# Kernel optimization log

Measured on AMD Instinct MI355X. Metric: run time of the kernel, lower is better.

Reference implementation:

```python
import jax, jax.numpy as jnp
import numpy as np


def setup_inputs() -> dict:
    key = jax.random.key(0)
    ks = jax.random.split(key, 5)
    B, S, D, E, H = 8, 4096, 512, 4, 64
    x = jax.random.normal(ks[0], (B, S, D), dtype=jnp.float32)
    router_w = jax.random.normal(ks[1], (D, E), dtype=jnp.float32) * 0.02
    router_b = jnp.zeros((E,), dtype=jnp.float32)
    w1 = jax.random.normal(ks[2], (E, D, H), dtype=jnp.float32) * 0.02
    b1 = jnp.zeros((E, H), dtype=jnp.float32)
    w2 = jax.random.normal(ks[3], (E, H, D), dtype=jnp.float32) * 0.02
    b2 = jnp.zeros((E, D), dtype=jnp.float32)
    return {"x": x, "router_w": router_w, "router_b": router_b,
            "w1": w1, "b1": b1, "w2": w2, "b2": b2}


def reference(x, router_w, router_b, w1, b1, w2, b2):
    # Router: softmax over experts. weights: [B, S, E]
    weights = jax.nn.softmax(jnp.einsum('bsd,de->bse', x, router_w) + router_b, axis=-1)
    # All experts run densely on every token (batched over the E axis).
    # h: [B, S, E, H]; TF Dense(activation='gelu') uses exact (non-tanh) gelu.
    h = jax.nn.gelu(jnp.einsum('bsd,edh->bseh', x, w1) + b1, approximate=False)
    # expert outputs: [B, S, E, D]; Dropout is identity at inference.
    expert_out = jnp.einsum('bseh,ehd->bsed', h, w2) + b2
    # weighted sum over experts -> [B, S, D]
    return jnp.sum(expert_out * weights[..., None], axis=2)
```

## Files before the change

kernel.cpp:

```cpp
#include <hip/hip_runtime.h>
#include <hip/hip_bf16.h>
#include <math.h>


typedef short v8s  __attribute__((ext_vector_type(8)));
typedef float v16f __attribute__((ext_vector_type(16)));

#define XS 520
#define HS 296

__device__ __forceinline__ unsigned short f2bf(float f) {
    unsigned int u = __builtin_bit_cast(unsigned int, f);
    u += 0x7fffu + ((u >> 16) & 1u);
    return (unsigned short)(u >> 16);
}
__device__ __forceinline__ float gelu_fast(float v) {
    float s  = v * 0.70710678118f;
    float xa = fabsf(s);
    float t  = 1.0f / (1.0f + 0.3275911f * xa);
    float poly = t * (0.254829592f + t * (-0.284496736f + t * (1.421413741f +
                 t * (-1.453152027f + t * 1.061405429f))));
    float er = copysignf(1.0f - poly * __expf(-xa * xa), s);
    return 0.5f * v * (1.0f + er);
}

__global__ void moe_prep(const float* __restrict__ w1,
                         const float* __restrict__ w2,
                         const float* __restrict__ b2,
                         const float* __restrict__ rw,
                         unsigned short* __restrict__ w1p,
                         unsigned short* __restrict__ w2p,
                         unsigned short* __restrict__ rp) {
    int idx = blockIdx.x * 256 + threadIdx.x;
    if (idx < 131072) {
        int block = idx >> 9, within = idx & 511;
        int kstep = block >> 3, cb = block & 7;
        int n = within >> 4, kl = within & 15;
        int k = kstep * 16 + kl;
        int col = cb * 32 + n;
        int e = col >> 6, h = col & 63;
        w1p[idx] = f2bf(w1[(e * 512 + k) * 64 + h]);
    } else if (idx < 131072 + 147456) {
        int op = idx - 131072;
        int block = op >> 9, within = op & 511;
        int kstep = block >> 4, cb = block & 15;
        int n = within >> 4, kl = within & 15;
        int k = kstep * 16 + kl;
        int d = cb * 32 + n;
        float v = 0.f;
        if (k < 256) {
            int e = k >> 6, h = k & 63;
            v = w2[(e * 64 + h) * 512 + d];
        } else if (k < 260) {
            v = b2[(k - 256) * 512 + d];
        }
        w2p[op] = f2bf(v);
    } else if (idx < 131072 + 147456 + 16384) {
        int op = idx - (131072 + 147456);
        int kstep = op >> 9, within = op & 511;
        int n = within >> 4, kl = within & 15;
        int k = kstep * 16 + kl;
        float v = (n < 4) ? rw[k * 4 + n] : 0.f;
        rp[op] = f2bf(v);
    }
}

__global__ __launch_bounds__(256, 2)
void moe_main(const float* __restrict__ x,
              const float* __restrict__ rb,
              const float* __restrict__ b1,
              const unsigned short* __restrict__ w1p,
              const unsigned short* __restrict__ w2p,
              const unsigned short* __restrict__ rp,
              float* __restrict__ out) {
    __shared__ __align__(16) unsigned short lx[64 * XS];
    __shared__ float lw[64 * 4];

    const int tid  = threadIdx.x;
    const int lane = tid & 63, wv = tid >> 6;
    const int ln = lane & 31, hi = lane >> 5;
    const long t0 = (long)blockIdx.x * 64;

    const float4* xt = (const float4*)(x + t0 * 512);
    #pragma unroll
    for (int it = 0; it < 32; ++it) {
        int F = it * 256 + tid;
        int row = F >> 7, c4 = F & 127;
        float4 v = xt[F];
        unsigned int p0 = (unsigned int)f2bf(v.x) | ((unsigned int)f2bf(v.y) << 16);
        unsigned int p1 = (unsigned int)f2bf(v.z) | ((unsigned int)f2bf(v.w) << 16);
        *(uint2*)&lx[row * XS + c4 * 4] = make_uint2(p0, p1);
    }
    __syncthreads();

    v16f acc1[2][2];
    v16f accR;
    #pragma unroll
    for (int j = 0; j < 16; ++j) accR[j] = 0.f;
    #pragma unroll
    for (int mt = 0; mt < 2; ++mt)
        #pragma unroll
        for (int nt = 0; nt < 2; ++nt)
            #pragma unroll
            for (int j = 0; j < 16; ++j) acc1[mt][nt][j] = 0.f;

    const unsigned short* w1b = w1p + (size_t)(wv * 2) * 512 + ln * 16 + hi * 8;
    const unsigned short* rpb = rp + ln * 16 + hi * 8;

    for (int ks = 0; ks < 32; ++ks) {
        v8s a0 = *(const v8s*)(const void*)&lx[ln * XS + ks * 16 + hi * 8];
        v8s a1 = *(const v8s*)(const void*)&lx[(32 + ln) * XS + ks * 16 + hi * 8];
        v8s b0 = *(const v8s*)(const void*)&w1b[(size_t)ks * 4096];
        v8s b1f = *(const v8s*)(const void*)&w1b[(size_t)ks * 4096 + 512];
        if (wv < 2) {
            v8s br = *(const v8s*)(const void*)&rpb[ks * 512];
            v8s ar = (wv == 0) ? a0 : a1;
            accR = __builtin_amdgcn_mfma_f32_32x32x16_bf16(ar, br, accR, 0, 0, 0);
        }
        acc1[0][0] = __builtin_amdgcn_mfma_f32_32x32x16_bf16(a0, b0, acc1[0][0], 0, 0, 0);
        acc1[0][1] = __builtin_amdgcn_mfma_f32_32x32x16_bf16(a0, b1f, acc1[0][1], 0, 0, 0);
        acc1[1][0] = __builtin_amdgcn_mfma_f32_32x32x16_bf16(a1, b0, acc1[1][0], 0, 0, 0);
        acc1[1][1] = __builtin_amdgcn_mfma_f32_32x32x16_bf16(a1, b1f, acc1[1][1], 0, 0, 0);
    }

    if (wv < 2) {
        float rbv = rb[ln & 3];
        #pragma unroll
        for (int j = 0; j < 16; ++j) {
            float v = accR[j] + rbv;
            float m = fmaxf(v, __shfl_xor(v, 1));
            m = fmaxf(m, __shfl_xor(m, 2));
            float e = __expf(v - m);
            float s = e + __shfl_xor(e, 1);
            s += __shfl_xor(s, 2);
            if (ln < 4) {
                int row = 32 * wv + (j & 3) + 8 * (j >> 2) + 4 * hi;
                lw[row * 4 + ln] = e / s;
            }
        }
    }
    __syncthreads();

    {
        float b1v[2];
        #pragma unroll
        for (int nt = 0; nt < 2; ++nt) b1v[nt] = b1[wv * 64 + 32 * nt + ln];
        #pragma unroll
        for (int mt = 0; mt < 2; ++mt) {
            #pragma unroll
            for (int j = 0; j < 16; ++j) {
                int row = 32 * mt + (j & 3) + 8 * (j >> 2) + 4 * hi;
                float wt = lw[row * 4 + wv];
                #pragma unroll
                for (int nt = 0; nt < 2; ++nt) {
                    float v = acc1[mt][nt][j] + b1v[nt];
                    float g = gelu_fast(v) * wt;
                    lx[row * HS + wv * 64 + 32 * nt + ln] = f2bf(g);
                }
            }
        }
        int r = tid >> 2, e = tid & 3;
        lx[r * HS + 256 + e] = f2bf(lw[tid]);
        #pragma unroll
        for (int i = 0; i < 7; ++i)
            lx[r * HS + 260 + e + 4 * i] = 0;
    }
    __syncthreads();

    v16f acc2[2][4];
    #pragma unroll
    for (int mt = 0; mt < 2; ++mt)
        #pragma unroll
        for (int nt = 0; nt < 4; ++nt)
            #pragma unroll
            for (int j = 0; j < 16; ++j) acc2[mt][nt][j] = 0.f;

    const unsigned short* w2b = w2p + (size_t)(wv * 4) * 512 + ln * 16 + hi * 8;

    for (int ks = 0; ks < 18; ++ks) {
        v8s a0 = *(const v8s*)(const void*)&lx[ln * HS + ks * 16 + hi * 8];
        v8s a1 = *(const v8s*)(const void*)&lx[(32 + ln) * HS + ks * 16 + hi * 8];
        v8s b[4];
        #pragma unroll
        for (int nt = 0; nt < 4; ++nt)
            b[nt] = *(const v8s*)(const void*)&w2b[(size_t)ks * 8192 + nt * 512];
        #pragma unroll
        for (int nt = 0; nt < 4; ++nt) {
            acc2[0][nt] = __builtin_amdgcn_mfma_f32_32x32x16_bf16(a0, b[nt], acc2[0][nt], 0, 0, 0);
            acc2[1][nt] = __builtin_amdgcn_mfma_f32_32x32x16_bf16(a1, b[nt], acc2[1][nt], 0, 0, 0);
        }
    }

    float* ot = out + t0 * 512;
    #pragma unroll
    for (int mt = 0; mt < 2; ++mt)
        #pragma unroll
        for (int nt = 0; nt < 4; ++nt)
            #pragma unroll
            for (int j = 0; j < 16; ++j) {
                int row = 32 * mt + (j & 3) + 8 * (j >> 2) + 4 * hi;
                int col = 128 * wv + 32 * nt + ln;
                ot[row * 512 + col] = acc2[mt][nt][j];
            }
}

extern "C" void kernel_launch(void* const* d_in, const int* in_sizes, int n_in,
                              void* d_out, int out_size, void* d_ws, size_t ws_size,
                              hipStream_t stream) {
    const float* x  = (const float*)d_in[0];
    const float* rw = (const float*)d_in[1];
    const float* rb = (const float*)d_in[2];
    const float* w1 = (const float*)d_in[3];
    const float* b1 = (const float*)d_in[4];
    const float* w2 = (const float*)d_in[5];
    const float* b2 = (const float*)d_in[6];

    unsigned short* w1p = (unsigned short*)d_ws;
    unsigned short* w2p = w1p + 131072;
    unsigned short* rp  = w2p + 147456;

    moe_prep<<<1152, 256, 0, stream>>>(w1, w2, b2, rw, w1p, w2p, rp);
    moe_main<<<512, 256, 0, stream>>>(x, rb, b1, w1p, w2p, rp, (float*)d_out);
}
```

Measured before the change: 148.5 us.

## Double-buffer weight loads in both GEMMs and split output GEMM into two passes

Both MFMA loops now software-pipeline the global weight-fragment loads, prefetching the next k-step into a second register set while the current one computes. The second GEMM is split into two passes of two N-tiles each, halving the live accumulator registers so the prefetch buffers fit. The fp32-to-bf16 conversion of x uses the packed hardware instruction v_cvt_pk_bf16_f32 instead of manual rounding. The two-pass split reloads the A fragments from LDS twice, and the router weights are now loaded by every wave, not only the two that use them.

Result: faster. 145.4 us (-2.1%).

```diff
diff --git a/kernel.cpp b/kernel.cpp
--- a/kernel.cpp
+++ b/kernel.cpp
@@ -13,6 +13,11 @@
     unsigned int u = __builtin_bit_cast(unsigned int, f);
     u += 0x7fffu + ((u >> 16) & 1u);
     return (unsigned short)(u >> 16);
+}
+__device__ __forceinline__ unsigned int cvtpk(float lo, float hi) {
+    unsigned int r;
+    asm("v_cvt_pk_bf16_f32 %0, %1, %2" : "=v"(r) : "v"(lo), "v"(hi));
+    return r;
 }
 __device__ __forceinline__ float gelu_fast(float v) {
     float s  = v * 0.70710678118f;
@@ -87,9 +92,7 @@
         int F = it * 256 + tid;
         int row = F >> 7, c4 = F & 127;
         float4 v = xt[F];
-        unsigned int p0 = (unsigned int)f2bf(v.x) | ((unsigned int)f2bf(v.y) << 16);
-        unsigned int p1 = (unsigned int)f2bf(v.z) | ((unsigned int)f2bf(v.w) << 16);
-        *(uint2*)&lx[row * XS + c4 * 4] = make_uint2(p0, p1);
+        *(uint2*)&lx[row * XS + c4 * 4] = make_uint2(cvtpk(v.x, v.y), cvtpk(v.z, v.w));
     }
     __syncthreads();
 
@@ -107,20 +110,34 @@
     const unsigned short* w1b = w1p + (size_t)(wv * 2) * 512 + ln * 16 + hi * 8;
     const unsigned short* rpb = rp + ln * 16 + hi * 8;
 
-    for (int ks = 0; ks < 32; ++ks) {
-        v8s a0 = *(const v8s*)(const void*)&lx[ln * XS + ks * 16 + hi * 8];
-        v8s a1 = *(const v8s*)(const void*)&lx[(32 + ln) * XS + ks * 16 + hi * 8];
-        v8s b0 = *(const v8s*)(const void*)&w1b[(size_t)ks * 4096];
-        v8s b1f = *(const v8s*)(const void*)&w1b[(size_t)ks * 4096 + 512];
-        if (wv < 2) {
-            v8s br = *(const v8s*)(const void*)&rpb[ks * 512];
-            v8s ar = (wv == 0) ? a0 : a1;
-            accR = __builtin_amdgcn_mfma_f32_32x32x16_bf16(ar, br, accR, 0, 0, 0);
-        }
-        acc1[0][0] = __builtin_amdgcn_mfma_f32_32x32x16_bf16(a0, b0, acc1[0][0], 0, 0, 0);
-        acc1[0][1] = __builtin_amdgcn_mfma_f32_32x32x16_bf16(a0, b1f, acc1[0][1], 0, 0, 0);
-        acc1[1][0] = __builtin_amdgcn_mfma_f32_32x32x16_bf16(a1, b0, acc1[1][0], 0, 0, 0);
-        acc1[1][1] = __builtin_amdgcn_mfma_f32_32x32x16_bf16(a1, b1f, acc1[1][1], 0, 0, 0);
+    #define LD1(B0, B1, BR, ks) do {                                               \
+        B0 = *(const v8s*)(const void*)&w1b[(size_t)(ks) * 4096];                  \
+        B1 = *(const v8s*)(const void*)&w1b[(size_t)(ks) * 4096 + 512];            \
+        BR = *(const v8s*)(const void*)&rpb[(ks) * 512];                           \
+    } while (0)
+
+    #define MM1(B0, B1, BR, ks) do {                                               \
+        v8s a0_ = *(const v8s*)(const void*)&lx[ln * XS + (ks) * 16 + hi * 8];     \
+        v8s a1_ = *(const v8s*)(const void*)&lx[(32 + ln) * XS + (ks) * 16 + hi * 8]; \
+        if (wv < 2) {                                                              \
+            v8s ar_ = (wv == 0) ? a0_ : a1_;                                       \
+            accR = __builtin_amdgcn_mfma_f32_32x32x16_bf16(ar_, BR, accR, 0, 0, 0);\
+        }                                                                          \
+        acc1[0][0] = __builtin_amdgcn_mfma_f32_32x32x16_bf16(a0_, B0, acc1[0][0], 0, 0, 0); \
+        acc1[0][1] = __builtin_amdgcn_mfma_f32_32x32x16_bf16(a0_, B1, acc1[0][1], 0, 0, 0); \
+        acc1[1][0] = __builtin_amdgcn_mfma_f32_32x32x16_bf16(a1_, B0, acc1[1][0], 0, 0, 0); \
+        acc1[1][1] = __builtin_amdgcn_mfma_f32_32x32x16_bf16(a1_, B1, acc1[1][1], 0, 0, 0); \
+    } while (0)
+
+    {
+        v8s pb0, pb1, pbr, qb0, qb1, qbr;
+        LD1(pb0, pb1, pbr, 0);
+        for (int kp = 0; kp < 16; ++kp) {
+            LD1(qb0, qb1, qbr, 2 * kp + 1);
+            MM1(pb0, pb1, pbr, 2 * kp);
+            if (kp < 15) LD1(pb0, pb1, pbr, 2 * kp + 2);
+            MM1(qb0, qb1, qbr, 2 * kp + 1);
+        }
     }
 
     if (wv < 2) {
@@ -167,41 +184,58 @@
     }
     __syncthreads();
 
-    v16f acc2[2][4];
-    #pragma unroll
-    for (int mt = 0; mt < 2; ++mt)
-        #pragma unroll
-        for (int nt = 0; nt < 4; ++nt)
-            #pragma unroll
-            for (int j = 0; j < 16; ++j) acc2[mt][nt][j] = 0.f;
-
     const unsigned short* w2b = w2p + (size_t)(wv * 4) * 512 + ln * 16 + hi * 8;
-
-    for (int ks = 0; ks < 18; ++ks) {
-        v8s a0 = *(const v8s*)(const void*)&lx[ln * HS + ks * 16 + hi * 8];
-        v8s a1 = *(const v8s*)(const void*)&lx[(32 + ln) * HS + ks * 16 + hi * 8];
-        v8s b[4];
-        #pragma unroll
-        for (int nt = 0; nt < 4; ++nt)
-            b[nt] = *(const v8s*)(const void*)&w2b[(size_t)ks * 8192 + nt * 512];
-        #pragma unroll
-        for (int nt = 0; nt < 4; ++nt) {
-            acc2[0][nt] = __builtin_amdgcn_mfma_f32_32x32x16_bf16(a0, b[nt], acc2[0][nt], 0, 0, 0);
-            acc2[1][nt] = __builtin_amdgcn_mfma_f32_32x32x16_bf16(a1, b[nt], acc2[1][nt], 0, 0, 0);
-        }
-    }
-
     float* ot = out + t0 * 512;
-    #pragma unroll
-    for (int mt = 0; mt < 2; ++mt)
-        #pragma unroll
-        for (int nt = 0; nt < 4; ++nt)
-            #pragma unroll
-            for (int j = 0; j < 16; ++j) {
-                int row = 32 * mt + (j & 3) + 8 * (j >> 2) + 4 * hi;
-                int col = 128 * wv + 32 * nt + ln;
-                ot[row * 512 + col] = acc2[mt][nt][j];
-            }
+
+    #define LD2(D0, D1, ks, poff) do {                                             \
+        D0 = *(const v8s*)(const void*)&w2b[(size_t)(ks) * 8192 + (poff)];         \
+        D1 = *(const v8s*)(const void*)&w2b[(size_t)(ks) * 8192 + (poff) + 512];   \
+    } while (0)
+
+    #define MM2(D0, D1, ks) do {                                                   \
+        v8s a0_ = *(const v8s*)(const void*)&lx[ln * HS + (ks) * 16 + hi * 8];     \
+        v8s a1_ = *(const v8s*)(const void*)&lx[(32 + ln) * HS + (ks) * 16 + hi * 8]; \
+        acc2[0][0] = __builtin_amdgcn_mfma_f32_32x32x16_bf16(a0_, D0, acc2[0][0], 0, 0, 0); \
+        acc2[0][1] = __builtin_amdgcn_mfma_f32_32x32x16_bf16(a0_, D1, acc2[0][1], 0, 0, 0); \
+        acc2[1][0] = __builtin_amdgcn_mfma_f32_32x32x16_bf16(a1_, D0, acc2[1][0], 0, 0, 0); \
+        acc2[1][1] = __builtin_amdgcn_mfma_f32_32x32x16_bf16(a1_, D1, acc2[1][1], 0, 0, 0); \
+    } while (0)
+
+    #pragma unroll 1
+    for (int pass = 0; pass < 2; ++pass) {
+        const int poff = pass * 1024;
+        v16f acc2[2][2];
+        #pragma unroll
+        for (int mt = 0; mt < 2; ++mt)
+            #pragma unroll
+            for (int nt = 0; nt < 2; ++nt)
+                #pragma unroll
+                for (int j = 0; j < 16; ++j) acc2[mt][nt][j] = 0.f;
+
+        v8s pd0, pd1, qd0, qd1;
+        LD2(pd0, pd1, 0, poff);
+        for (int kp = 0; kp < 9; ++kp) {
+            LD2(qd0, qd1, 2 * kp + 1, poff);
+            MM2(pd0, pd1, 2 * kp);
+            if (kp < 8) LD2(pd0, pd1, 2 * kp + 2, poff);
+            MM2(qd0, qd1, 2 * kp + 1);
+        }
+
+        #pragma unroll
+        for (int mt = 0; mt < 2; ++mt)
+            #pragma unroll
+            for (int nt = 0; nt < 2; ++nt)
+                #pragma unroll
+                for (int j = 0; j < 16; ++j) {
+                    int row = 32 * mt + (j & 3) + 8 * (j >> 2) + 4 * hi;
+                    int col = 128 * wv + 32 * (pass * 2 + nt) + ln;
+                    ot[row * 512 + col] = acc2[mt][nt][j];
+                }
+    }
+    #undef LD1
+    #undef MM1
+    #undef LD2
+    #undef MM2
 }
 
 extern "C" void kernel_launch(void* const* d_in, const int* in_sizes, int n_in,
```
